# Kernel tuning notes

Hardware: AMD Instinct MI355X
Metric: run time of the kernel (lower is better)

Reference implementation:

```python
import jax, jax.numpy as jnp
import numpy as np


def setup_inputs() -> dict:
    key = jax.random.key(0)
    k1, k2 = jax.random.split(key)
    h = jax.random.normal(k1, (8, 16, 64, 512), dtype=jnp.float32)
    M = jax.random.normal(k2, (20000, 512), dtype=jnp.float32)
    return {"h": h, "M": M}


def reference(h, M):
    # h: [B, T, X, R], M: [K, R]
    B, T, X, R = h.shape
    hf = h.reshape(-1, R)                      # [N, R]
    att = jax.nn.softmax(hf @ M.T, axis=1)     # [N, K], unscaled dot-product
    out = att @ M                              # [N, R]
    return out.reshape(B, T, X, R)
```

## Files before the change

kernel.cpp:

```cpp
#include <hip/hip_runtime.h>
#include <stdint.h>

#define NQ 8192
#define NK 20000
#define RD 512
#define NT 157
#define TS0 79

typedef float f32x4 __attribute__((ext_vector_type(4)));
typedef short s16x8 __attribute__((ext_vector_type(8)));

__device__ __forceinline__ unsigned short bf16_rn(float x) {
    uint32_t u = __float_as_uint(x);
    return (unsigned short)((u + 0x7FFFu + ((u >> 16) & 1)) >> 16);
}

__global__ void preconv_kernel(const float* __restrict__ M,
                               unsigned short* __restrict__ Mhi,
                               unsigned short* __restrict__ Mlo,
                               unsigned short* __restrict__ MT) {
    __shared__ float tilef[64 * 65];
    const int k0 = blockIdx.x * 64, r0 = blockIdx.y * 64;
    const int t = threadIdx.x;
#pragma unroll
    for (int i = 0; i < 16; i++) {
        int e = t + i * 256;
        int kr = e >> 6, cc = e & 63;
        int key = k0 + kr;
        if (key < NK) {
            float x = M[(size_t)key * RD + r0 + cc];
            uint32_t u = __float_as_uint(x);
            Mhi[(size_t)key * RD + r0 + cc] = (unsigned short)(u >> 16);
            Mlo[(size_t)key * RD + r0 + cc] = bf16_rn(x - __uint_as_float(u & 0xFFFF0000u));
            tilef[cc * 65 + kr] = x;
        }
    }
    __syncthreads();
#pragma unroll
    for (int i = 0; i < 16; i++) {
        int e = t + i * 256;
        int rr = e >> 6, kk = e & 63;
        int key = k0 + kk;
        if (key < NK) MT[(size_t)(r0 + rr) * NK + key] = bf16_rn(tilef[rr * 65 + kk]);
    }
}

__global__ __launch_bounds__(256, 2) void flash5_kernel(
        const float* __restrict__ h,
        const unsigned short* __restrict__ Mhi,
        const unsigned short* __restrict__ Mlo,
        const unsigned short* __restrict__ MT,
        float* __restrict__ out,
        float* __restrict__ Opart,
        float* __restrict__ mpart,
        float* __restrict__ lpart,
        int nsplit) {
    __shared__ unsigned short qbuf[32768];
    __shared__ unsigned short pbuf[8 * 512];
    __shared__ float smaxb[4 * 2 * 16];
    __shared__ float ssumb[4 * 2 * 16];

    const int tid = threadIdx.x;
    const int ch = tid >> 6, l = tid & 63;
    const int l15 = l & 15, q4 = l >> 4;
    const int kq = (l15 >> 3) & 1, jj = l15 & 7;

    int qb, split;
    if (nsplit == 2) { split = blockIdx.x & 1; qb = blockIdx.x >> 1; }
    else             { split = 0;              qb = blockIdx.x; }
    const int koff = (split == 0) ? 0 : TS0 * 128;
    const int ntl  = (nsplit == 2) ? ((split == 0) ? TS0 : (NT - TS0)) : NT;
    const int qbase = qb * 32;

#pragma unroll
    for (int i = 0; i < 8; i++) {
        int g = tid + i * 256;
        int row = g >> 6, s = (g >> 2) & 15, qg = g & 3;
        int strip = row >> 4, lrow = row & 15;
        const float* src = h + (size_t)(qbase + row) * RD + s * 32 + qg * 8;
        f32x4 a = *(const f32x4*)src;
        f32x4 b = *(const f32x4*)(src + 4);
        s16x8 hi8, lo8;
#pragma unroll
        for (int j = 0; j < 8; j++) {
            float x = (j < 4) ? a[j] : b[j - 4];
            uint32_t u = __float_as_uint(x);
            hi8[j] = (short)(u >> 16);
            lo8[j] = (short)bf16_rn(x - __uint_as_float(u & 0xFFFF0000u));
        }
        int off = ((strip * 16 + s) * 512 + (qg * 16 + lrow) * 8);
        *(s16x8*)&qbuf[off] = hi8;
        *(s16x8*)&qbuf[16384 + off] = lo8;
    }
    __syncthreads();

    f32x4 O[2][8];
#pragma unroll
    for (int st = 0; st < 2; st++)
#pragma unroll
        for (int ct = 0; ct < 8; ct++) O[st][ct] = 0.f;
    f32x4 m_run[2], l_run[2];
    m_run[0] = -3e38f; m_run[1] = -3e38f; l_run[0] = 0.f; l_run[1] = 0.f;

    s16x8 khq[2][2], klq[2][2];
    {
        const size_t b0 = (size_t)(koff + ch * 32 + l15) * RD + q4 * 8;
        const size_t b1 = b0 + (size_t)16 * RD;
        khq[0][0] = *(const s16x8*)(Mhi + b0);
        khq[0][1] = *(const s16x8*)(Mhi + b0 + 32);
        klq[0][0] = *(const s16x8*)(Mlo + b0);
        klq[0][1] = *(const s16x8*)(Mlo + b0 + 32);
        khq[1][0] = *(const s16x8*)(Mhi + b1);
        khq[1][1] = *(const s16x8*)(Mhi + b1 + 32);
        klq[1][0] = *(const s16x8*)(Mlo + b1);
        klq[1][1] = *(const s16x8*)(Mlo + b1 + 32);
    }

    for (int tile = 0; tile < ntl; tile++) {
        const size_t kbase0 = (size_t)(koff + tile * 128 + ch * 32 + l15) * RD + q4 * 8;
        const size_t kbase1 = kbase0 + (size_t)16 * RD;

        f32x4 C[2][2];
        C[0][0] = 0.f; C[0][1] = 0.f; C[1][0] = 0.f; C[1][1] = 0.f;
#pragma unroll
        for (int s = 0; s < 16; s++) {
            s16x8 kh0 = khq[0][s & 1], kl0 = klq[0][s & 1];
            s16x8 kh1 = khq[1][s & 1], kl1 = klq[1][s & 1];
            if (s < 14) {
                khq[0][s & 1] = *(const s16x8*)(Mhi + kbase0 + (s + 2) * 32);
                klq[0][s & 1] = *(const s16x8*)(Mlo + kbase0 + (s + 2) * 32);
                khq[1][s & 1] = *(const s16x8*)(Mhi + kbase1 + (s + 2) * 32);
                klq[1][s & 1] = *(const s16x8*)(Mlo + kbase1 + (s + 2) * 32);
            }
#pragma unroll
            for (int st = 0; st < 2; st++) {
                s16x8 qh = *(const s16x8*)&qbuf[(st * 16 + s) * 512 + l * 8];
                s16x8 ql = *(const s16x8*)&qbuf[16384 + (st * 16 + s) * 512 + l * 8];
                C[st][0] = __builtin_amdgcn_mfma_f32_16x16x32_bf16(qh, kh0, C[st][0], 0, 0, 0);
                C[st][1] = __builtin_amdgcn_mfma_f32_16x16x32_bf16(qh, kh1, C[st][1], 0, 0, 0);
                C[st][0] = __builtin_amdgcn_mfma_f32_16x16x32_bf16(ql, kh0, C[st][0], 0, 0, 0);
                C[st][1] = __builtin_amdgcn_mfma_f32_16x16x32_bf16(ql, kh1, C[st][1], 0, 0, 0);
                C[st][0] = __builtin_amdgcn_mfma_f32_16x16x32_bf16(qh, kl0, C[st][0], 0, 0, 0);
                C[st][1] = __builtin_amdgcn_mfma_f32_16x16x32_bf16(qh, kl1, C[st][1], 0, 0, 0);
            }
        }
        if (tile == ntl - 1) {
#pragma unroll
            for (int cb = 0; cb < 2; cb++) {
                int kg = koff + tile * 128 + ch * 32 + cb * 16 + l15;
                if (kg >= NK) { C[0][cb] = -3e38f; C[1][cb] = -3e38f; }
            }
        }

        f32x4 mx[2];
#pragma unroll
        for (int st = 0; st < 2; st++)
#pragma unroll
            for (int v = 0; v < 4; v++) mx[st][v] = fmaxf(C[st][0][v], C[st][1][v]);
#pragma unroll
        for (int d = 1; d < 16; d <<= 1) {
#pragma unroll
            for (int st = 0; st < 2; st++)
#pragma unroll
                for (int v = 0; v < 4; v++) mx[st][v] = fmaxf(mx[st][v], __shfl_xor(mx[st][v], d, 16));
        }
        if (l15 == 0) {
            *(f32x4*)&smaxb[(ch * 2 + 0) * 16 + q4 * 4] = mx[0];
            *(f32x4*)&smaxb[(ch * 2 + 1) * 16 + q4 * 4] = mx[1];
        }
        __syncthreads();
        f32x4 mnew[2]; mnew[0] = m_run[0]; mnew[1] = m_run[1];
#pragma unroll
        for (int cc = 0; cc < 4; cc++) {
#pragma unroll
            for (int st = 0; st < 2; st++) {
                f32x4 tv = *(const f32x4*)&smaxb[(cc * 2 + st) * 16 + q4 * 4];
#pragma unroll
                for (int v = 0; v < 4; v++) mnew[st][v] = fmaxf(mnew[st][v], tv[v]);
            }
        }
        f32x4 alpha[2];
#pragma unroll
        for (int st = 0; st < 2; st++)
#pragma unroll
            for (int v = 0; v < 4; v++) {
                alpha[st][v] = __expf(m_run[st][v] - mnew[st][v]);
                m_run[st][v] = mnew[st][v];
            }
        f32x4 ps[2]; ps[0] = 0.f; ps[1] = 0.f;
#pragma unroll
        for (int st = 0; st < 2; st++) {
#pragma unroll
            for (int cb = 0; cb < 2; cb++) {
#pragma unroll
                for (int v = 0; v < 4; v++) {
                    float p = __expf(C[st][cb][v] - mnew[st][v]);
                    ps[st][v] += p;
                    pbuf[(ch * 2 + st) * 512 + ((cb * 2 + kq) * 16 + q4 * 4 + v) * 8 + jj] = bf16_rn(p);
                }
            }
        }
#pragma unroll
        for (int d = 1; d < 16; d <<= 1) {
#pragma unroll
            for (int st = 0; st < 2; st++)
#pragma unroll
                for (int v = 0; v < 4; v++) ps[st][v] += __shfl_xor(ps[st][v], d, 16);
        }
        if (l15 == 0) {
            *(f32x4*)&ssumb[(ch * 2 + 0) * 16 + q4 * 4] = ps[0];
            *(f32x4*)&ssumb[(ch * 2 + 1) * 16 + q4 * 4] = ps[1];
        }
        __syncthreads();
        f32x4 ts[2]; ts[0] = 0.f; ts[1] = 0.f;
#pragma unroll
        for (int cc = 0; cc < 4; cc++) {
            ts[0] += *(const f32x4*)&ssumb[(cc * 2 + 0) * 16 + q4 * 4];
            ts[1] += *(const f32x4*)&ssumb[(cc * 2 + 1) * 16 + q4 * 4];
        }
#pragma unroll
        for (int st = 0; st < 2; st++)
#pragma unroll
            for (int v = 0; v < 4; v++) l_run[st][v] = l_run[st][v] * alpha[st][v] + ts[st][v];
#pragma unroll
        for (int st = 0; st < 2; st++)
#pragma unroll
            for (int ct = 0; ct < 8; ct++)
#pragma unroll
                for (int v = 0; v < 4; v++) O[st][ct][v] *= alpha[st][v];
        s16x8 pa[2][4];
#pragma unroll
        for (int st = 0; st < 2; st++)
#pragma unroll
            for (int sk = 0; sk < 4; sk++)
                pa[st][sk] = *(const s16x8*)&pbuf[((sk * 2 + st) * 512) + l * 8];

        if (tile < ntl - 1) {
            const size_t nb0 = (size_t)(koff + (tile + 1) * 128 + ch * 32 + l15) * RD + q4 * 8;
            const size_t nb1 = nb0 + (size_t)16 * RD;
            khq[0][0] = *(const s16x8*)(Mhi + nb0);
            khq[0][1] = *(const s16x8*)(Mhi + nb0 + 32);
            klq[0][0] = *(const s16x8*)(Mlo + nb0);
            klq[0][1] = *(const s16x8*)(Mlo + nb0 + 32);
            khq[1][0] = *(const s16x8*)(Mhi + nb1);
            khq[1][1] = *(const s16x8*)(Mhi + nb1 + 32);
            klq[1][0] = *(const s16x8*)(Mlo + nb1);
            klq[1][1] = *(const s16x8*)(Mlo + nb1 + 32);
        }

        const unsigned short* mtp = MT + (size_t)(ch * 128 + l15) * NK + koff + tile * 128 + q4 * 8;
#pragma unroll
        for (int ct = 0; ct < 8; ct++) {
            s16x8 btC[4];
#pragma unroll
            for (int sk = 0; sk < 4; sk++)
                btC[sk] = *(const s16x8*)(mtp + (size_t)ct * 16 * NK + sk * 32);
#pragma unroll
            for (int sk = 0; sk < 4; sk++) {
                O[0][ct] = __builtin_amdgcn_mfma_f32_16x16x32_bf16(pa[0][sk], btC[sk], O[0][ct], 0, 0, 0);
                O[1][ct] = __builtin_amdgcn_mfma_f32_16x16x32_bf16(pa[1][sk], btC[sk], O[1][ct], 0, 0, 0);
            }
        }
    }

    if (nsplit == 2) {
        float* Od = Opart + (size_t)split * NQ * RD;
#pragma unroll
        for (int st = 0; st < 2; st++)
#pragma unroll
            for (int ct = 0; ct < 8; ct++)
#pragma unroll
                for (int v = 0; v < 4; v++)
                    Od[(size_t)(qbase + st * 16 + q4 * 4 + v) * RD + ch * 128 + ct * 16 + l15] =
                        O[st][ct][v];
        if (ch == 0 && l15 == 0) {
#pragma unroll
            for (int st = 0; st < 2; st++)
#pragma unroll
                for (int v = 0; v < 4; v++) {
                    mpart[split * NQ + qbase + st * 16 + q4 * 4 + v] = m_run[st][v];
                    lpart[split * NQ + qbase + st * 16 + q4 * 4 + v] = l_run[st][v];
                }
        }
    } else {
#pragma unroll
        for (int st = 0; st < 2; st++)
#pragma unroll
            for (int ct = 0; ct < 8; ct++)
#pragma unroll
                for (int v = 0; v < 4; v++)
                    out[(size_t)(qbase + st * 16 + q4 * 4 + v) * RD + ch * 128 + ct * 16 + l15] =
                        O[st][ct][v] / l_run[st][v];
    }
}

__global__ __launch_bounds__(256) void combine_kernel(const float* __restrict__ Opart,
                                                      const float* __restrict__ mpart,
                                                      const float* __restrict__ lpart,
                                                      float* __restrict__ out) {
    const int t = threadIdx.x;
    const int row = blockIdx.x * 2 + (t >> 7);
    const int d = (t & 127) * 4;
    float m0 = mpart[row], m1 = mpart[NQ + row];
    float l0 = lpart[row], l1 = lpart[NQ + row];
    float m = fmaxf(m0, m1);
    float w0 = __expf(m0 - m), w1 = __expf(m1 - m);
    float inv = 1.f / (w0 * l0 + w1 * l1);
    f32x4 o0 = *(const f32x4*)&Opart[(size_t)row * RD + d];
    f32x4 o1 = *(const f32x4*)&Opart[(size_t)NQ * RD + (size_t)row * RD + d];
    f32x4 r;
#pragma unroll
    for (int v = 0; v < 4; v++) r[v] = (o0[v] * w0 + o1[v] * w1) * inv;
    *(f32x4*)&out[(size_t)row * RD + d] = r;
}

__global__ __launch_bounds__(256) void naive_kernel(const float* __restrict__ h,
                                                    const float* __restrict__ M,
                                                    float* __restrict__ out) {
    __shared__ float hs[16 * 520];
    __shared__ float ms[8 * 520];
    __shared__ float sdot[2][128];
    __shared__ float sm[16], sl[16], sal[16], sp[16][8];
    const int t = threadIdx.x;
    const int qbase = blockIdx.x * 16;
#pragma unroll
    for (int i = 0; i < 32; i++) {
        int e = t + i * 256;
        int row = e >> 9, col = e & 511;
        hs[row * 520 + col] = h[(size_t)(qbase + row) * RD + col];
    }
    if (t < 16) { sm[t] = -3e38f; sl[t] = 0.f; }
    float Oacc[32];
#pragma unroll
    for (int i = 0; i < 32; i++) Oacc[i] = 0.f;
    const int q = t >> 4;
    const int eb = (t & 15) * 32;

    for (int k0 = 0; k0 < NK; k0 += 8) {
        __syncthreads();
#pragma unroll
        for (int i = 0; i < 16; i++) {
            int e = t + i * 256;
            if (e < 4096) {
                int kk = e >> 9, col = e & 511;
                ms[kk * 520 + col] = M[(size_t)(k0 + kk) * RD + col];
            }
        }
        __syncthreads();
        {
            int pair = t & 127, half = t >> 7;
            int qq = pair & 15, kk = pair >> 4;
            const float* hp = &hs[qq * 520 + half * 256];
            const float* mp = &ms[kk * 520 + half * 256];
            float acc = 0.f;
#pragma unroll 8
            for (int e = 0; e < 256; e++) acc += hp[e] * mp[e];
            sdot[half][pair] = acc;
        }
        __syncthreads();
        if (t < 16) {
            int qq = t;
            float s8[8];
#pragma unroll
            for (int kk = 0; kk < 8; kk++) s8[kk] = sdot[0][qq + 16 * kk] + sdot[1][qq + 16 * kk];
            float mn = sm[qq];
#pragma unroll
            for (int kk = 0; kk < 8; kk++) mn = fmaxf(mn, s8[kk]);
            float al = __expf(sm[qq] - mn);
            float addl = 0.f;
#pragma unroll
            for (int kk = 0; kk < 8; kk++) { float p = __expf(s8[kk] - mn); sp[qq][kk] = p; addl += p; }
            sm[qq] = mn; sl[qq] = sl[qq] * al + addl; sal[qq] = al;
        }
        __syncthreads();
        {
            float al = sal[q];
#pragma unroll
            for (int i = 0; i < 32; i++) Oacc[i] *= al;
#pragma unroll
            for (int kk = 0; kk < 8; kk++) {
                float p = sp[q][kk];
                const float* mp = &ms[kk * 520 + eb];
#pragma unroll
                for (int i = 0; i < 32; i++) Oacc[i] += p * mp[i];
            }
        }
    }
    __syncthreads();
    float inv = 1.f / sl[q];
#pragma unroll
    for (int i = 0; i < 32; i++) out[(size_t)(qbase + q) * RD + eb + i] = Oacc[i] * inv;
}

extern "C" void kernel_launch(void* const* d_in, const int* in_sizes, int n_in,
                              void* d_out, int out_size, void* d_ws, size_t ws_size,
                              hipStream_t stream) {
    const float* h = (const float*)d_in[0];
    const float* M = (const float*)d_in[1];
    float* out = (float*)d_out;
    const size_t seg = (size_t)NK * RD;
    const size_t base_bytes = (seg * 3ull + 8192ull) * 2ull;
    const size_t opart_bytes = 2ull * NQ * RD * 4ull;
    const size_t stat_bytes = 2ull * 2ull * NQ * 4ull;
    const size_t need_split = base_bytes + opart_bytes + stat_bytes;

    if (ws_size >= base_bytes) {
        unsigned short* Mhi = (unsigned short*)d_ws;
        unsigned short* Mlo = Mhi + seg;
        unsigned short* MT  = Mlo + seg;
        float* Opart = (float*)((char*)d_ws + base_bytes);
        float* mpart = Opart + 2ull * NQ * RD;
        float* lpart = mpart + 2ull * NQ;
        preconv_kernel<<<dim3(313, 8), 256, 0, stream>>>(M, Mhi, Mlo, MT);
        if (ws_size >= need_split) {
            flash5_kernel<<<512, 256, 0, stream>>>(h, Mhi, Mlo, MT, out, Opart, mpart, lpart, 2);
            combine_kernel<<<NQ / 2, 256, 0, stream>>>(Opart, mpart, lpart, out);
        } else {
            flash5_kernel<<<256, 256, 0, stream>>>(h, Mhi, Mlo, MT, out, Opart, mpart, lpart, 1);
        }
    } else {
        naive_kernel<<<512, 256, 0, stream>>>(h, M, out);
    }
}
```

Before: 1.672 ms.

## Deepen K prefetch ring across tiles and double-buffer MT loads in PV loop

Replaces the two-deep per-tile K prefetch with a four-deep rotating register ring whose addresses run continuously across tile boundaries, so the first K slices of the next tile are already in flight. The first MT slices are issued before the softmax reduction, and the PV loop double-buffers MT loads two column tiles ahead. __syncthreads is replaced by a waitcnt-plus-s_barrier inline asm, and a barrier is added at the end of each tile. This targets global-load latency stalls, at the cost of more live VGPRs, which could cause spills or lower occupancy under launch_bounds(256,2).

```diff
diff --git a/kernel.cpp b/kernel.cpp
--- a/kernel.cpp
+++ b/kernel.cpp
@@ -13,6 +13,10 @@
 __device__ __forceinline__ unsigned short bf16_rn(float x) {
     uint32_t u = __float_as_uint(x);
     return (unsigned short)((u + 0x7FFFu + ((u >> 16) & 1)) >> 16);
+}
+
+__device__ __forceinline__ void lds_barrier() {
+    asm volatile("s_waitcnt lgkmcnt(0)\n\ts_barrier" ::: "memory");
 }
 
 __global__ void preconv_kernel(const float* __restrict__ M,
@@ -45,7 +49,7 @@
     }
 }
 
-__global__ __launch_bounds__(256, 2) void flash5_kernel(
+__global__ __launch_bounds__(256, 2) void flash6_kernel(
         const float* __restrict__ h,
         const unsigned short* __restrict__ Mhi,
         const unsigned short* __restrict__ Mlo,
@@ -70,7 +74,25 @@
     else             { split = 0;              qb = blockIdx.x; }
     const int koff = (split == 0) ? 0 : TS0 * 128;
     const int ntl  = (nsplit == 2) ? ((split == 0) ? TS0 : (NT - TS0)) : NT;
+    const int total_ks = ntl * 16;
     const int qbase = qb * 32;
+
+    const size_t base_w = (size_t)(ch * 32 + l15) * RD + q4 * 8;
+    auto kaddr = [&](int g, int cb) -> size_t {
+        if (g >= total_ks) g = total_ks - 1;
+        int t2 = g >> 4, s2 = g & 15;
+        return (size_t)(koff + t2 * 128) * RD + (size_t)s2 * 32 + base_w + (size_t)cb * (16 * RD);
+    };
+
+    s16x8 kh[2][4], kl[2][4];
+#pragma unroll
+    for (int i = 0; i < 4; i++) {
+        size_t a0 = kaddr(i, 0), a1 = kaddr(i, 1);
+        kh[0][i] = *(const s16x8*)(Mhi + a0);
+        kl[0][i] = *(const s16x8*)(Mlo + a0);
+        kh[1][i] = *(const s16x8*)(Mhi + a1);
+        kl[1][i] = *(const s16x8*)(Mlo + a1);
+    }
 
 #pragma unroll
     for (int i = 0; i < 8; i++) {
@@ -92,7 +114,7 @@
         *(s16x8*)&qbuf[off] = hi8;
         *(s16x8*)&qbuf[16384 + off] = lo8;
     }
-    __syncthreads();
+    lds_barrier();
 
     f32x4 O[2][8];
 #pragma unroll
@@ -102,35 +124,21 @@
     f32x4 m_run[2], l_run[2];
     m_run[0] = -3e38f; m_run[1] = -3e38f; l_run[0] = 0.f; l_run[1] = 0.f;
 
-    s16x8 khq[2][2], klq[2][2];
-    {
-        const size_t b0 = (size_t)(koff + ch * 32 + l15) * RD + q4 * 8;
-        const size_t b1 = b0 + (size_t)16 * RD;
-        khq[0][0] = *(const s16x8*)(Mhi + b0);
-        khq[0][1] = *(const s16x8*)(Mhi + b0 + 32);
-        klq[0][0] = *(const s16x8*)(Mlo + b0);
-        klq[0][1] = *(const s16x8*)(Mlo + b0 + 32);
-        khq[1][0] = *(const s16x8*)(Mhi + b1);
-        khq[1][1] = *(const s16x8*)(Mhi + b1 + 32);
-        klq[1][0] = *(const s16x8*)(Mlo + b1);
-        klq[1][1] = *(const s16x8*)(Mlo + b1 + 32);
-    }
-
     for (int tile = 0; tile < ntl; tile++) {
-        const size_t kbase0 = (size_t)(koff + tile * 128 + ch * 32 + l15) * RD + q4 * 8;
-        const size_t kbase1 = kbase0 + (size_t)16 * RD;
-
         f32x4 C[2][2];
         C[0][0] = 0.f; C[0][1] = 0.f; C[1][0] = 0.f; C[1][1] = 0.f;
 #pragma unroll
         for (int s = 0; s < 16; s++) {
-            s16x8 kh0 = khq[0][s & 1], kl0 = klq[0][s & 1];
-            s16x8 kh1 = khq[1][s & 1], kl1 = klq[1][s & 1];
-            if (s < 14) {
-                khq[0][s & 1] = *(const s16x8*)(Mhi + kbase0 + (s + 2) * 32);
-                klq[0][s & 1] = *(const s16x8*)(Mlo + kbase0 + (s + 2) * 32);
-                khq[1][s & 1] = *(const s16x8*)(Mhi + kbase1 + (s + 2) * 32);
-                klq[1][s & 1] = *(const s16x8*)(Mlo + kbase1 + (s + 2) * 32);
+            const int sl = s & 3;
+            s16x8 kh0 = kh[0][sl], kl0 = kl[0][sl];
+            s16x8 kh1 = kh[1][sl], kl1 = kl[1][sl];
+            {
+                int g = tile * 16 + s + 4;
+                size_t a0 = kaddr(g, 0), a1 = kaddr(g, 1);
+                kh[0][sl] = *(const s16x8*)(Mhi + a0);
+                kl[0][sl] = *(const s16x8*)(Mlo + a0);
+                kh[1][sl] = *(const s16x8*)(Mhi + a1);
+                kl[1][sl] = *(const s16x8*)(Mlo + a1);
             }
 #pragma unroll
             for (int st = 0; st < 2; st++) {
@@ -152,6 +160,14 @@
             }
         }
 
+        const unsigned short* mtp = MT + (size_t)(ch * 128 + l15) * NK + koff + tile * 128 + q4 * 8;
+        s16x8 bt[2][4];
+#pragma unroll
+        for (int sk = 0; sk < 4; sk++) {
+            bt[0][sk] = *(const s16x8*)(mtp + sk * 32);
+            bt[1][sk] = *(const s16x8*)(mtp + (size_t)16 * NK + sk * 32);
+        }
+
         f32x4 mx[2];
 #pragma unroll
         for (int st = 0; st < 2; st++)
@@ -168,7 +184,7 @@
             *(f32x4*)&smaxb[(ch * 2 + 0) * 16 + q4 * 4] = mx[0];
             *(f32x4*)&smaxb[(ch * 2 + 1) * 16 + q4 * 4] = mx[1];
         }
-        __syncthreads();
+        lds_barrier();
         f32x4 mnew[2]; mnew[0] = m_run[0]; mnew[1] = m_run[1];
 #pragma unroll
         for (int cc = 0; cc < 4; cc++) {
@@ -211,7 +227,7 @@
             *(f32x4*)&ssumb[(ch * 2 + 0) * 16 + q4 * 4] = ps[0];
             *(f32x4*)&ssumb[(ch * 2 + 1) * 16 + q4 * 4] = ps[1];
         }
-        __syncthreads();
+        lds_barrier();
         f32x4 ts[2]; ts[0] = 0.f; ts[1] = 0.f;
 #pragma unroll
         for (int cc = 0; cc < 4; cc++) {
@@ -235,32 +251,24 @@
             for (int sk = 0; sk < 4; sk++)
                 pa[st][sk] = *(const s16x8*)&pbuf[((sk * 2 + st) * 512) + l * 8];
 
-        if (tile < ntl - 1) {
-            const size_t nb0 = (size_t)(koff + (tile + 1) * 128 + ch * 32 + l15) * RD + q4 * 8;
-            const size_t nb1 = nb0 + (size_t)16 * RD;
-            khq[0][0] = *(const s16x8*)(Mhi + nb0);
-            khq[0][1] = *(const s16x8*)(Mhi + nb0 + 32);
-            klq[0][0] = *(const s16x8*)(Mlo + nb0);
-            klq[0][1] = *(const s16x8*)(Mlo + nb0 + 32);
-            khq[1][0] = *(const s16x8*)(Mhi + nb1);
-            khq[1][1] = *(const s16x8*)(Mhi + nb1 + 32);
-            klq[1][0] = *(const s16x8*)(Mlo + nb1);
-            klq[1][1] = *(const s16x8*)(Mlo + nb1 + 32);
-        }
-
-        const unsigned short* mtp = MT + (size_t)(ch * 128 + l15) * NK + koff + tile * 128 + q4 * 8;
 #pragma unroll
         for (int ct = 0; ct < 8; ct++) {
-            s16x8 btC[4];
-#pragma unroll
-            for (int sk = 0; sk < 4; sk++)
-                btC[sk] = *(const s16x8*)(mtp + (size_t)ct * 16 * NK + sk * 32);
-#pragma unroll
-            for (int sk = 0; sk < 4; sk++) {
-                O[0][ct] = __builtin_amdgcn_mfma_f32_16x16x32_bf16(pa[0][sk], btC[sk], O[0][ct], 0, 0, 0);
-                O[1][ct] = __builtin_amdgcn_mfma_f32_16x16x32_bf16(pa[1][sk], btC[sk], O[1][ct], 0, 0, 0);
-            }
-        }
+            s16x8 b0 = bt[ct & 1][0], b1 = bt[ct & 1][1], b2 = bt[ct & 1][2], b3 = bt[ct & 1][3];
+            if (ct < 6) {
+#pragma unroll
+                for (int sk = 0; sk < 4; sk++)
+                    bt[ct & 1][sk] = *(const s16x8*)(mtp + (size_t)(ct + 2) * 16 * NK + sk * 32);
+            }
+            O[0][ct] = __builtin_amdgcn_mfma_f32_16x16x32_bf16(pa[0][0], b0, O[0][ct], 0, 0, 0);
+            O[1][ct] = __builtin_amdgcn_mfma_f32_16x16x32_bf16(pa[1][0], b0, O[1][ct], 0, 0, 0);
+            O[0][ct] = __builtin_amdgcn_mfma_f32_16x16x32_bf16(pa[0][1], b1, O[0][ct], 0, 0, 0);
+            O[1][ct] = __builtin_amdgcn_mfma_f32_16x16x32_bf16(pa[1][1], b1, O[1][ct], 0, 0, 0);
+            O[0][ct] = __builtin_amdgcn_mfma_f32_16x16x32_bf16(pa[0][2], b2, O[0][ct], 0, 0, 0);
+            O[1][ct] = __builtin_amdgcn_mfma_f32_16x16x32_bf16(pa[1][2], b2, O[1][ct], 0, 0, 0);
+            O[0][ct] = __builtin_amdgcn_mfma_f32_16x16x32_bf16(pa[0][3], b3, O[0][ct], 0, 0, 0);
+            O[1][ct] = __builtin_amdgcn_mfma_f32_16x16x32_bf16(pa[1][3], b3, O[1][ct], 0, 0, 0);
+        }
+        lds_barrier();
     }
 
     if (nsplit == 2) {
@@ -413,10 +421,10 @@
         float* lpart = mpart + 2ull * NQ;
         preconv_kernel<<<dim3(313, 8), 256, 0, stream>>>(M, Mhi, Mlo, MT);
         if (ws_size >= need_split) {
-            flash5_kernel<<<512, 256, 0, stream>>>(h, Mhi, Mlo, MT, out, Opart, mpart, lpart, 2);
+            flash6_kernel<<<512, 256, 0, stream>>>(h, Mhi, Mlo, MT, out, Opart, mpart, lpart, 2);
             combine_kernel<<<NQ / 2, 256, 0, stream>>>(Opart, mpart, lpart, out);
         } else {
-            flash5_kernel<<<256, 256, 0, stream>>>(h, Mhi, Mlo, MT, out, Opart, mpart, lpart, 1);
+            flash6_kernel<<<256, 256, 0, stream>>>(h, Mhi, Mlo, MT, out, Opart, mpart, lpart, 1);
         }
     } else {
         naive_kernel<<<512, 256, 0, stream>>>(h, M, out);
```

Result: faster. 1.588 ms (-5.0%).
